# Optimization experiments

Measured on AMD Instinct MI355X. Metric: run time of the kernel, lower is better.

## Reference

```python
import jax, jax.numpy as jnp
import numpy as np

D_MODEL = 512
NUM_HEADS = 8
VOCAB = 32000
B, TQ, TS = 4, 512, 512


def setup_inputs() -> dict:
    key = jax.random.key(0)
    ks = jax.random.split(key, 12)
    s = 1.0 / np.sqrt(D_MODEL)
    inp = {
        "src_vocab_size": VOCAB,
        "dec_output": jax.random.normal(ks[0], (B, TQ, D_MODEL), jnp.float32),
        "enc_output": jax.random.normal(ks[1], (B, TS, D_MODEL), jnp.float32),
        "src": jax.random.randint(ks[2], (B, TS), 0, VOCAB),
        "p1": jax.random.uniform(ks[3], (B, TQ, VOCAB), jnp.float32),
        # fcQ: d_model -> d_model (xavier)
        "WfcQ": jax.random.normal(ks[4], (D_MODEL, D_MODEL), jnp.float32) * s,
        "bfcQ": jnp.zeros((D_MODEL,), jnp.float32),
        # MHA query / key projections (V and output proj skipped in copy mode)
        "Wq": jax.random.normal(ks[5], (D_MODEL, D_MODEL), jnp.float32) * s,
        "bq": jnp.zeros((D_MODEL,), jnp.float32),
        "Wk": jax.random.normal(ks[6], (D_MODEL, D_MODEL), jnp.float32) * s,
        "bk": jnp.zeros((D_MODEL,), jnp.float32),
        # fcw: d_model -> 1 gate
        "Wfcw": jax.random.normal(ks[7], (1, D_MODEL), jnp.float32) * s,
        "bfcw": jnp.zeros((1,), jnp.float32),
    }
    return inp


def reference(src_vocab_size, dec_output, enc_output, src, p1,
              WfcQ, bfcQ, Wq, bq, Wk, bk, Wfcw, bfcw):
    b, tq, d = dec_output.shape
    h = NUM_HEADS
    dh = d // h
    # copy_query = fcQ(dec_output)
    cq = dec_output @ WfcQ.T + bfcQ
    # per-head Q, K projections
    Q = (cq @ Wq.T + bq).reshape(b, tq, h, dh).transpose(0, 2, 1, 3)          # [b,h,tq,dh]
    K = (enc_output @ Wk.T + bk).reshape(b, -1, h, dh).transpose(0, 2, 1, 3)  # [b,h,ts,dh]
    scale = 1.0 / jnp.sqrt(jnp.asarray(dh, dec_output.dtype))
    scores = jnp.einsum('bhqd,bhkd->bhqk', Q, K) * scale
    attn = jax.nn.softmax(scores, axis=-1).mean(axis=1)  # [b,tq,ts] head-averaged
    # attn @ one_hot(src, vocab)  ==  scatter-add of attn weights by src token id
    def scatter_copy(a, s):  # a: [tq,ts], s: [ts]
        return jax.ops.segment_sum(a.T, s, num_segments=src_vocab_size).T  # [tq,vocab]
    a_output = jax.vmap(scatter_copy)(attn, src)  # [b,tq,vocab]
    p2 = jax.nn.softmax(a_output, axis=-1)
    w = jax.nn.sigmoid(dec_output @ Wfcw.T + bfcw)  # [b,tq,1]
    return p2 * w + (1.0 - w) * p1
```

## Files before the change

### kernel.cpp

```cpp
#include <hip/hip_runtime.h>

constexpr int BATCH = 4;
constexpr int SEQ   = 512;
constexpr int DM    = 512;
constexpr int NH    = 8;
constexpr int NV    = 32000;
constexpr int NROWS = BATCH * SEQ;

typedef short short8 __attribute__((ext_vector_type(8)));
typedef float floatx4 __attribute__((ext_vector_type(4)));

__device__ __forceinline__ float wave_reduce_max(float v) {
#pragma unroll
  for (int o = 32; o > 0; o >>= 1) v = fmaxf(v, __shfl_down(v, o, 64));
  return v;
}
__device__ __forceinline__ float wave_reduce_sum(float v) {
#pragma unroll
  for (int o = 32; o > 0; o >>= 1) v += __shfl_down(v, o, 64);
  return v;
}
__device__ __forceinline__ unsigned short f2bf(float f) {
  unsigned u = __float_as_uint(f);
  u += 0x7FFFu + ((u >> 16) & 1u);
  return (unsigned short)(u >> 16);
}
__device__ __forceinline__ float bf2f(unsigned short b) {
  return __uint_as_float(((unsigned)b) << 16);
}

__global__ __launch_bounds__(256)
void convert_bf16_kernel(const float* __restrict__ in, unsigned short* __restrict__ out, int n4) {
  const int i = blockIdx.x * 256 + threadIdx.x;
  if (i < n4) {
    const float4 v = ((const float4*)in)[i];
    ushort4 o;
    o.x = f2bf(v.x); o.y = f2bf(v.y); o.z = f2bf(v.z); o.w = f2bf(v.w);
    ((ushort4*)out)[i] = o;
  }
}

__global__ __launch_bounds__(256)
void wfold_kernel(const float* __restrict__ Wq, const float* __restrict__ WfcQ,
                  unsigned short* __restrict__ Wqc) {
  __shared__ float As[16][68];
  __shared__ float Bs[16][68];
  const int tid = threadIdx.x, tx = tid & 15, ty = tid >> 4;
  const int m0 = blockIdx.y << 6, n0 = blockIdx.x << 6;
  const int r = tid >> 2, c = (tid & 3) << 2;
  float acc[4][4] = {};
  for (int k0 = 0; k0 < DM; k0 += 16) {
    const float4 av = *(const float4*)(Wq + (size_t)(m0 + r) * DM + k0 + c);
    As[c + 0][r] = av.x; As[c + 1][r] = av.y; As[c + 2][r] = av.z; As[c + 3][r] = av.w;
    const float4 bv = *(const float4*)(WfcQ + (size_t)(k0 + ty) * DM + n0 + (tx << 2));
    *(float4*)(&Bs[ty][tx << 2]) = bv;
    __syncthreads();
#pragma unroll
    for (int kk = 0; kk < 16; ++kk) {
      const float4 a4 = *(const float4*)(&As[kk][ty << 2]);
      const float4 b4 = *(const float4*)(&Bs[kk][tx << 2]);
      const float a[4] = {a4.x, a4.y, a4.z, a4.w};
      const float b[4] = {b4.x, b4.y, b4.z, b4.w};
#pragma unroll
      for (int i = 0; i < 4; ++i)
#pragma unroll
        for (int j = 0; j < 4; ++j) acc[i][j] = fmaf(a[i], b[j], acc[i][j]);
    }
    __syncthreads();
  }
#pragma unroll
  for (int i = 0; i < 4; ++i)
#pragma unroll
    for (int j = 0; j < 4; ++j)
      Wqc[(size_t)(m0 + (ty << 2) + i) * DM + n0 + (tx << 2) + j] = f2bf(acc[i][j]);
}

__global__ __launch_bounds__(512)
void bias_fold_kernel(const float* __restrict__ Wq, const float* __restrict__ bfcQ,
                      const float* __restrict__ bq, float* __restrict__ bq2) {
  const int tid = threadIdx.x, h = tid >> 6, l = tid & 63;
  const int n = blockIdx.x * 8 + h;
  float s = 0.f;
#pragma unroll
  for (int t = 0; t < 8; ++t) {
    const int j = l + 64 * t;
    s = fmaf(Wq[(size_t)n * DM + j], bfcQ[j], s);
  }
  s = wave_reduce_sum(s);
  if (l == 0) bq2[n] = bq[n] + s;
}

__global__ __launch_bounds__(256)
void gemm_mfma_kernel(const unsigned short* __restrict__ A0, const unsigned short* __restrict__ W0,
                      const float* __restrict__ b0, unsigned short* __restrict__ C0,
                      const unsigned short* __restrict__ A1, const unsigned short* __restrict__ W1,
                      const float* __restrict__ b1, unsigned short* __restrict__ C1) {
  const unsigned short* A; const unsigned short* W; const float* bias; unsigned short* C;
  if (blockIdx.z == 0) { A = A0; W = W0; bias = b0; C = C0; }
  else                 { A = A1; W = W1; bias = b1; C = C1; }
  const int m0 = blockIdx.y << 6, n0 = blockIdx.x << 6;
  __shared__ __align__(16) unsigned short As[64 * 72];
  __shared__ __align__(16) unsigned short Ws[64 * 72];
  const int tid = threadIdx.x;
  const int wv = tid >> 6, l = tid & 63;
  const int lm = l & 15, lq = l >> 4;
  floatx4 acc[4] = {};
  for (int k0 = 0; k0 < DM; k0 += 64) {
#pragma unroll
    for (int i = 0; i < 2; ++i) {
      const int ch = tid + (i << 8);
      const int row = ch >> 3, c8 = (ch & 7) << 3;
      *(int4*)(&As[row * 72 + c8]) = *(const int4*)(A + (size_t)(m0 + row) * DM + k0 + c8);
      *(int4*)(&Ws[row * 72 + c8]) = *(const int4*)(W + (size_t)(n0 + row) * DM + k0 + c8);
    }
    __syncthreads();
#pragma unroll
    for (int ks = 0; ks < 64; ks += 32) {
      const short8 a = *(const short8*)(&As[(16 * wv + lm) * 72 + ks + lq * 8]);
#pragma unroll
      for (int c = 0; c < 4; ++c) {
        const short8 b = *(const short8*)(&Ws[(16 * c + lm) * 72 + ks + lq * 8]);
        acc[c] = __builtin_amdgcn_mfma_f32_16x16x32_bf16(a, b, acc[c], 0, 0, 0);
      }
    }
    __syncthreads();
  }
#pragma unroll
  for (int c = 0; c < 4; ++c) {
    const int col = n0 + 16 * c + lm;
    const float bv = bias[col];
#pragma unroll
    for (int r = 0; r < 4; ++r) {
      const int row = m0 + 16 * wv + lq * 4 + r;
      C[(size_t)row * DM + col] = f2bf(acc[c][r] + bv);
    }
  }
}

__global__ __launch_bounds__(256)
void scores_mfma_kernel(const unsigned short* __restrict__ Q, const unsigned short* __restrict__ Kk,
                        unsigned short* __restrict__ scores) {
  const int bh = blockIdx.z, bb = bh >> 3, h = bh & 7;
  const int tq0 = blockIdx.y << 6, ts0 = blockIdx.x << 6;
  __shared__ __align__(16) unsigned short Qs[64 * 72];
  __shared__ __align__(16) unsigned short Ks[64 * 72];
  const int tid = threadIdx.x;
  const int wv = tid >> 6, l = tid & 63;
  const int lm = l & 15, lq = l >> 4;
#pragma unroll
  for (int i = 0; i < 2; ++i) {
    const int ch = tid + (i << 8);
    const int row = ch >> 3, c8 = (ch & 7) << 3;
    *(int4*)(&Qs[row * 72 + c8]) =
        *(const int4*)(Q + (size_t)(bb * SEQ + tq0 + row) * DM + h * 64 + c8);
    *(int4*)(&Ks[row * 72 + c8]) =
        *(const int4*)(Kk + (size_t)(bb * SEQ + ts0 + row) * DM + h * 64 + c8);
  }
  __syncthreads();
  floatx4 acc[4] = {};
#pragma unroll
  for (int ks = 0; ks < 64; ks += 32) {
    const short8 a = *(const short8*)(&Qs[(16 * wv + lm) * 72 + ks + lq * 8]);
#pragma unroll
    for (int c = 0; c < 4; ++c) {
      const short8 b = *(const short8*)(&Ks[(16 * c + lm) * 72 + ks + lq * 8]);
      acc[c] = __builtin_amdgcn_mfma_f32_16x16x32_bf16(a, b, acc[c], 0, 0, 0);
    }
  }
#pragma unroll
  for (int c = 0; c < 4; ++c) {
    const int ts = ts0 + 16 * c + lm;
#pragma unroll
    for (int r = 0; r < 4; ++r) {
      const int tq = tq0 + 16 * wv + lq * 4 + r;
      scores[((size_t)bh * SEQ + tq) * SEQ + ts] = f2bf(acc[c][r] * 0.125f);
    }
  }
}

__global__ void build_map_kernel(const int* __restrict__ src, int* __restrict__ map) {
  const int bb = blockIdx.x, ts = threadIdx.x;
  const int v = src[bb * SEQ + ts];
  atomicCAS(&map[(size_t)bb * NV + v], -1, ts);
}

__global__ __launch_bounds__(512)
void softmax_fused_kernel(const unsigned short* __restrict__ scores, const int* __restrict__ src,
                          const int* __restrict__ map, const float* __restrict__ dec,
                          const float* __restrict__ Wfcw, const float* __restrict__ bfcw,
                          float* __restrict__ expa, float* __restrict__ row_a,
                          float* __restrict__ row_b) {
  __shared__ float hp[8 * 520];
  __shared__ float aslot[512];
  __shared__ float r1[8], r2[8];
  const int row = blockIdx.x, bb = row >> 9, tq = row & 511;
  const int tid = threadIdx.x, h = tid >> 6, l = tid & 63;
  aslot[tid] = 0.f;
  const unsigned short* srow = scores + ((size_t)(bb * NH + h) * SEQ + tq) * SEQ;
  union { int4 v; unsigned short u[8]; } U;
  U.v = *(const int4*)(srow + 8 * l);
  float s[8];
#pragma unroll
  for (int i = 0; i < 8; ++i) s[i] = bf2f(U.u[i]);
  float m = s[0];
#pragma unroll
  for (int i = 1; i < 8; ++i) m = fmaxf(m, s[i]);
  m = wave_reduce_max(m);
  m = __shfl(m, 0, 64);
  float e[8], sum = 0.f;
#pragma unroll
  for (int i = 0; i < 8; ++i) { e[i] = __expf(s[i] - m); sum += e[i]; }
  sum = wave_reduce_sum(sum);
  sum = __shfl(sum, 0, 64);
  const float inv = 1.f / sum;
  float4 p0, p1v;
  p0.x = e[0] * inv; p0.y = e[1] * inv; p0.z = e[2] * inv; p0.w = e[3] * inv;
  p1v.x = e[4] * inv; p1v.y = e[5] * inv; p1v.z = e[6] * inv; p1v.w = e[7] * inv;
  *(float4*)(&hp[h * 520 + 8 * l])     = p0;
  *(float4*)(&hp[h * 520 + 8 * l + 4]) = p1v;
  __syncthreads();
  float a = 0.f;
#pragma unroll
  for (int h2 = 0; h2 < 8; ++h2) a += hp[h2 * 520 + tid];
  a *= 0.125f;
  const int sv = src[bb * SEQ + tid];
  const int rep = map[(size_t)bb * NV + sv];
  atomicAdd(&aslot[rep], a);
  __syncthreads();
  const float ev = __expf(aslot[tid]);
  expa[(size_t)row * SEQ + tid] = ev;
  const float d = dec[(size_t)row * DM + tid] * Wfcw[tid];
  float es = wave_reduce_sum(ev);
  float ds = wave_reduce_sum(d);
  if (l == 0) { r1[h] = es; r2[h] = ds; }
  __syncthreads();
  if (tid == 0) {
    float esum = 0.f, dsum = bfcw[0];
#pragma unroll
    for (int i = 0; i < 8; ++i) { esum += r1[i]; dsum += r2[i]; }
    const float w = 1.f / (1.f + __expf(-dsum));
    row_a[row] = 1.f - w;
    row_b[row] = w / ((float)(NV - SEQ) + esum);
  }
}

__global__ __launch_bounds__(256)
void final_kernel(const float* __restrict__ p1, const int* __restrict__ map,
                  const float* __restrict__ expa, const float* __restrict__ row_a,
                  const float* __restrict__ row_b, float* __restrict__ out) {
  const size_t g = (size_t)blockIdx.x * 256 + threadIdx.x;
  const int row = (int)(g / (NV / 4));
  const int q4  = (int)(g % (NV / 4));
  const int bb = row >> 9;
  const float4 p = ((const float4*)p1)[g];
  const int4 m = *(const int4*)(map + (size_t)bb * NV + (q4 << 2));
  const float ra = row_a[row], rb = row_b[row];
  const float* ea = expa + (size_t)row * SEQ;
  const float e0 = (m.x >= 0) ? ea[m.x] : 1.f;
  const float e1 = (m.y >= 0) ? ea[m.y] : 1.f;
  const float e2 = (m.z >= 0) ? ea[m.z] : 1.f;
  const float e3 = (m.w >= 0) ? ea[m.w] : 1.f;
  float4 o;
  o.x = fmaf(ra, p.x, rb * e0);
  o.y = fmaf(ra, p.y, rb * e1);
  o.z = fmaf(ra, p.z, rb * e2);
  o.w = fmaf(ra, p.w, rb * e3);
  ((float4*)out)[g] = o;
}

extern "C" void kernel_launch(void* const* d_in, const int* in_sizes, int n_in,
                              void* d_out, int out_size, void* d_ws, size_t ws_size,
                              hipStream_t stream) {
  const float* dec  = (const float*)d_in[1];
  const float* enc  = (const float*)d_in[2];
  const int*   src  = (const int*)d_in[3];
  const float* p1   = (const float*)d_in[4];
  const float* WfcQ = (const float*)d_in[5];
  const float* bfcQ = (const float*)d_in[6];
  const float* Wq   = (const float*)d_in[7];
  const float* bq   = (const float*)d_in[8];
  const float* Wk   = (const float*)d_in[9];
  const float* bk   = (const float*)d_in[10];
  const float* Wfcw = (const float*)d_in[11];
  const float* bfcw = (const float*)d_in[12];
  float* out = (float*)d_out;

  char* ws = (char*)d_ws;
  int*            map     = (int*)(ws);
  unsigned short* dec_bf  = (unsigned short*)(ws + (size_t)( 1 << 20));
  unsigned short* enc_bf  = (unsigned short*)(ws + (size_t)( 3 << 20));
  unsigned short* wk_bf   = (unsigned short*)(ws + (size_t)( 5 << 20));
  unsigned short* wqc_bf  = (unsigned short*)(ws + (size_t)( 5 << 20) + (512 << 10));
  float*          bq2     = (float*)(ws + (size_t)( 6 << 20));
  float*          row_a   = (float*)(ws + (size_t)( 6 << 20) + (64 << 10));
  float*          row_b   = (float*)(ws + (size_t)( 6 << 20) + (128 << 10));
  unsigned short* qlin_bf = (unsigned short*)(ws + (size_t)( 7 << 20));
  unsigned short* klin_bf = (unsigned short*)(ws + (size_t)( 9 << 20));
  float*          expa    = (float*)(ws + (size_t)(11 << 20));
  unsigned short* scores  = (unsigned short*)(ws + (size_t)(16 << 20));

  hipMemsetAsync(map, 0xFF, (size_t)BATCH * NV * sizeof(int), stream);
  build_map_kernel<<<BATCH, SEQ, 0, stream>>>(src, map);

  convert_bf16_kernel<<<1024, 256, 0, stream>>>(dec, dec_bf, NROWS * DM / 4);
  convert_bf16_kernel<<<1024, 256, 0, stream>>>(enc, enc_bf, NROWS * DM / 4);
  convert_bf16_kernel<<<256, 256, 0, stream>>>(Wk, wk_bf, DM * DM / 4);

  wfold_kernel<<<dim3(8, 8), 256, 0, stream>>>(Wq, WfcQ, wqc_bf);
  bias_fold_kernel<<<64, 512, 0, stream>>>(Wq, bfcQ, bq, bq2);

  gemm_mfma_kernel<<<dim3(8, 32, 2), 256, 0, stream>>>(
      dec_bf, wqc_bf, bq2, qlin_bf, enc_bf, wk_bf, bk, klin_bf);

  scores_mfma_kernel<<<dim3(8, 8, 32), 256, 0, stream>>>(qlin_bf, klin_bf, scores);

  softmax_fused_kernel<<<NROWS, 512, 0, stream>>>(scores, src, map, dec, Wfcw, bfcw,
                                                  expa, row_a, row_b);

  final_kernel<<<(NROWS * (NV / 4)) / 256, 256, 0, stream>>>(p1, map, expa, row_a, row_b, out);
}
```

Baseline: 520.7 us.

## Merge prep kernels, stage GEMM/score stores via LDS, streamline final pass

```diff
diff --git a/kernel.cpp b/kernel.cpp
--- a/kernel.cpp
+++ b/kernel.cpp
@@ -9,6 +9,7 @@
 
 typedef short short8 __attribute__((ext_vector_type(8)));
 typedef float floatx4 __attribute__((ext_vector_type(4)));
+typedef float floatv4 __attribute__((ext_vector_type(4)));
 
 __device__ __forceinline__ float wave_reduce_max(float v) {
 #pragma unroll
@@ -30,64 +31,75 @@
 }
 
 __global__ __launch_bounds__(256)
-void convert_bf16_kernel(const float* __restrict__ in, unsigned short* __restrict__ out, int n4) {
-  const int i = blockIdx.x * 256 + threadIdx.x;
-  if (i < n4) {
+void prep_kernel(const float* __restrict__ dec, const float* __restrict__ enc,
+                 const float* __restrict__ Wk,
+                 unsigned short* __restrict__ dec_bf, unsigned short* __restrict__ enc_bf,
+                 unsigned short* __restrict__ wk_bf,
+                 const int* __restrict__ src, int* __restrict__ map,
+                 const float* __restrict__ Wq, const float* __restrict__ WfcQ,
+                 unsigned short* __restrict__ wqc_bf,
+                 const float* __restrict__ bfcQ, const float* __restrict__ bq,
+                 float* __restrict__ bq2) {
+  __shared__ float As[16][68];
+  __shared__ float Bs[16][68];
+  const int b = blockIdx.x, tid = threadIdx.x;
+  if (b < 64) {
+    const int m0 = (b >> 3) << 6, n0 = (b & 7) << 6;
+    const int tx = tid & 15, ty = tid >> 4;
+    const int r = tid >> 2, c = (tid & 3) << 2;
+    float acc[4][4] = {};
+    for (int k0 = 0; k0 < DM; k0 += 16) {
+      const float4 av = *(const float4*)(Wq + (size_t)(m0 + r) * DM + k0 + c);
+      As[c + 0][r] = av.x; As[c + 1][r] = av.y; As[c + 2][r] = av.z; As[c + 3][r] = av.w;
+      const float4 bv = *(const float4*)(WfcQ + (size_t)(k0 + ty) * DM + n0 + (tx << 2));
+      *(float4*)(&Bs[ty][tx << 2]) = bv;
+      __syncthreads();
+#pragma unroll
+      for (int kk = 0; kk < 16; ++kk) {
+        const float4 a4 = *(const float4*)(&As[kk][ty << 2]);
+        const float4 b4 = *(const float4*)(&Bs[kk][tx << 2]);
+        const float a[4] = {a4.x, a4.y, a4.z, a4.w};
+        const float bb[4] = {b4.x, b4.y, b4.z, b4.w};
+#pragma unroll
+        for (int i = 0; i < 4; ++i)
+#pragma unroll
+          for (int j = 0; j < 4; ++j) acc[i][j] = fmaf(a[i], bb[j], acc[i][j]);
+      }
+      __syncthreads();
+    }
+#pragma unroll
+    for (int i = 0; i < 4; ++i)
+#pragma unroll
+      for (int j = 0; j < 4; ++j)
+        wqc_bf[(size_t)(m0 + (ty << 2) + i) * DM + n0 + (tx << 2) + j] = f2bf(acc[i][j]);
+  } else if (b < 2368) {
+    const int cb = b - 64;
+    const float* in; unsigned short* outp; int i;
+    if (cb < 1024)      { in = dec; outp = dec_bf; i = cb * 256 + tid; }
+    else if (cb < 2048) { in = enc; outp = enc_bf; i = (cb - 1024) * 256 + tid; }
+    else                { in = Wk;  outp = wk_bf;  i = (cb - 2048) * 256 + tid; }
     const float4 v = ((const float4*)in)[i];
     ushort4 o;
     o.x = f2bf(v.x); o.y = f2bf(v.y); o.z = f2bf(v.z); o.w = f2bf(v.w);
-    ((ushort4*)out)[i] = o;
-  }
-}
-
-__global__ __launch_bounds__(256)
-void wfold_kernel(const float* __restrict__ Wq, const float* __restrict__ WfcQ,
-                  unsigned short* __restrict__ Wqc) {
-  __shared__ float As[16][68];
-  __shared__ float Bs[16][68];
-  const int tid = threadIdx.x, tx = tid & 15, ty = tid >> 4;
-  const int m0 = blockIdx.y << 6, n0 = blockIdx.x << 6;
-  const int r = tid >> 2, c = (tid & 3) << 2;
-  float acc[4][4] = {};
-  for (int k0 = 0; k0 < DM; k0 += 16) {
-    const float4 av = *(const float4*)(Wq + (size_t)(m0 + r) * DM + k0 + c);
-    As[c + 0][r] = av.x; As[c + 1][r] = av.y; As[c + 2][r] = av.z; As[c + 3][r] = av.w;
-    const float4 bv = *(const float4*)(WfcQ + (size_t)(k0 + ty) * DM + n0 + (tx << 2));
-    *(float4*)(&Bs[ty][tx << 2]) = bv;
-    __syncthreads();
-#pragma unroll
-    for (int kk = 0; kk < 16; ++kk) {
-      const float4 a4 = *(const float4*)(&As[kk][ty << 2]);
-      const float4 b4 = *(const float4*)(&Bs[kk][tx << 2]);
-      const float a[4] = {a4.x, a4.y, a4.z, a4.w};
-      const float b[4] = {b4.x, b4.y, b4.z, b4.w};
-#pragma unroll
-      for (int i = 0; i < 4; ++i)
-#pragma unroll
-        for (int j = 0; j < 4; ++j) acc[i][j] = fmaf(a[i], b[j], acc[i][j]);
-    }
-    __syncthreads();
-  }
-#pragma unroll
-  for (int i = 0; i < 4; ++i)
-#pragma unroll
-    for (int j = 0; j < 4; ++j)
-      Wqc[(size_t)(m0 + (ty << 2) + i) * DM + n0 + (tx << 2) + j] = f2bf(acc[i][j]);
-}
-
-__global__ __launch_bounds__(512)
-void bias_fold_kernel(const float* __restrict__ Wq, const float* __restrict__ bfcQ,
-                      const float* __restrict__ bq, float* __restrict__ bq2) {
-  const int tid = threadIdx.x, h = tid >> 6, l = tid & 63;
-  const int n = blockIdx.x * 8 + h;
-  float s = 0.f;
-#pragma unroll
-  for (int t = 0; t < 8; ++t) {
-    const int j = l + 64 * t;
-    s = fmaf(Wq[(size_t)n * DM + j], bfcQ[j], s);
-  }
-  s = wave_reduce_sum(s);
-  if (l == 0) bq2[n] = bq[n] + s;
+    ((ushort4*)outp)[i] = o;
+  } else if (b < 2372) {
+    const int bb = b - 2368;
+    const int v0 = src[bb * SEQ + tid];
+    atomicCAS(&map[(size_t)bb * NV + v0], -1, tid);
+    const int v1 = src[bb * SEQ + tid + 256];
+    atomicCAS(&map[(size_t)bb * NV + v1], -1, tid + 256);
+  } else {
+    const int h = tid >> 6, l = tid & 63;
+    const int n = (b - 2372) * 4 + h;
+    float s = 0.f;
+#pragma unroll
+    for (int t = 0; t < 8; ++t) {
+      const int j = l + 64 * t;
+      s = fmaf(Wq[(size_t)n * DM + j], bfcQ[j], s);
+    }
+    s = wave_reduce_sum(s);
+    if (l == 0) bq2[n] = bq[n] + s;
+  }
 }
 
 __global__ __launch_bounds__(256)
@@ -127,13 +139,17 @@
   }
 #pragma unroll
   for (int c = 0; c < 4; ++c) {
-    const int col = n0 + 16 * c + lm;
-    const float bv = bias[col];
-#pragma unroll
-    for (int r = 0; r < 4; ++r) {
-      const int row = m0 + 16 * wv + lq * 4 + r;
-      C[(size_t)row * DM + col] = f2bf(acc[c][r] + bv);
-    }
+    const float bv = bias[n0 + 16 * c + lm];
+#pragma unroll
+    for (int r = 0; r < 4; ++r)
+      As[(16 * wv + lq * 4 + r) * 72 + 16 * c + lm] = f2bf(acc[c][r] + bv);
+  }
+  __syncthreads();
+#pragma unroll
+  for (int i = 0; i < 2; ++i) {
+    const int idx = tid + (i << 8);
+    const int row = idx >> 3, c8 = (idx & 7) << 3;
+    *(int4*)(C + (size_t)(m0 + row) * DM + n0 + c8) = *(const int4*)(&As[row * 72 + c8]);
   }
 }
 
@@ -167,21 +183,20 @@
       acc[c] = __builtin_amdgcn_mfma_f32_16x16x32_bf16(a, b, acc[c], 0, 0, 0);
     }
   }
-#pragma unroll
-  for (int c = 0; c < 4; ++c) {
-    const int ts = ts0 + 16 * c + lm;
-#pragma unroll
-    for (int r = 0; r < 4; ++r) {
-      const int tq = tq0 + 16 * wv + lq * 4 + r;
-      scores[((size_t)bh * SEQ + tq) * SEQ + ts] = f2bf(acc[c][r] * 0.125f);
-    }
-  }
-}
-
-__global__ void build_map_kernel(const int* __restrict__ src, int* __restrict__ map) {
-  const int bb = blockIdx.x, ts = threadIdx.x;
-  const int v = src[bb * SEQ + ts];
-  atomicCAS(&map[(size_t)bb * NV + v], -1, ts);
+  __syncthreads();
+#pragma unroll
+  for (int c = 0; c < 4; ++c)
+#pragma unroll
+    for (int r = 0; r < 4; ++r)
+      Qs[(16 * wv + lq * 4 + r) * 72 + 16 * c + lm] = f2bf(acc[c][r] * 0.125f);
+  __syncthreads();
+#pragma unroll
+  for (int i = 0; i < 2; ++i) {
+    const int idx = tid + (i << 8);
+    const int row = idx >> 3, c8 = (idx & 7) << 3;
+    *(int4*)(scores + ((size_t)bh * SEQ + tq0 + row) * SEQ + ts0 + c8) =
+        *(const int4*)(&Qs[row * 72 + c8]);
+  }
 }
 
 __global__ __launch_bounds__(512)
@@ -244,28 +259,32 @@
   }
 }
 
-__global__ __launch_bounds__(256)
+__global__ __launch_bounds__(320)
 void final_kernel(const float* __restrict__ p1, const int* __restrict__ map,
                   const float* __restrict__ expa, const float* __restrict__ row_a,
                   const float* __restrict__ row_b, float* __restrict__ out) {
-  const size_t g = (size_t)blockIdx.x * 256 + threadIdx.x;
-  const int row = (int)(g / (NV / 4));
-  const int q4  = (int)(g % (NV / 4));
-  const int bb = row >> 9;
-  const float4 p = ((const float4*)p1)[g];
+  const int row = blockIdx.y;
+  const int q4  = blockIdx.x * 320 + threadIdx.x;
+  const int bb  = row >> 9;
+  const size_t g = (size_t)row * (NV / 4) + q4;
+  const floatv4 p = __builtin_nontemporal_load((const floatv4*)p1 + g);
   const int4 m = *(const int4*)(map + (size_t)bb * NV + (q4 << 2));
   const float ra = row_a[row], rb = row_b[row];
   const float* ea = expa + (size_t)row * SEQ;
-  const float e0 = (m.x >= 0) ? ea[m.x] : 1.f;
-  const float e1 = (m.y >= 0) ? ea[m.y] : 1.f;
-  const float e2 = (m.z >= 0) ? ea[m.z] : 1.f;
-  const float e3 = (m.w >= 0) ? ea[m.w] : 1.f;
-  float4 o;
+  const float t0 = ea[m.x & 511];
+  const float t1 = ea[m.y & 511];
+  const float t2 = ea[m.z & 511];
+  const float t3 = ea[m.w & 511];
+  const float e0 = (m.x >= 0) ? t0 : 1.f;
+  const float e1 = (m.y >= 0) ? t1 : 1.f;
+  const float e2 = (m.z >= 0) ? t2 : 1.f;
+  const float e3 = (m.w >= 0) ? t3 : 1.f;
+  floatv4 o;
   o.x = fmaf(ra, p.x, rb * e0);
   o.y = fmaf(ra, p.y, rb * e1);
   o.z = fmaf(ra, p.z, rb * e2);
   o.w = fmaf(ra, p.w, rb * e3);
-  ((float4*)out)[g] = o;
+  __builtin_nontemporal_store(o, (floatv4*)out + g);
 }
 
 extern "C" void kernel_launch(void* const* d_in, const int* in_sizes, int n_in,
@@ -300,14 +319,9 @@
   unsigned short* scores  = (unsigned short*)(ws + (size_t)(16 << 20));
 
   hipMemsetAsync(map, 0xFF, (size_t)BATCH * NV * sizeof(int), stream);
-  build_map_kernel<<<BATCH, SEQ, 0, stream>>>(src, map);
-
-  convert_bf16_kernel<<<1024, 256, 0, stream>>>(dec, dec_bf, NROWS * DM / 4);
-  convert_bf16_kernel<<<1024, 256, 0, stream>>>(enc, enc_bf, NROWS * DM / 4);
-  convert_bf16_kernel<<<256, 256, 0, stream>>>(Wk, wk_bf, DM * DM / 4);
-
-  wfold_kernel<<<dim3(8, 8), 256, 0, stream>>>(Wq, WfcQ, wqc_bf);
-  bias_fold_kernel<<<64, 512, 0, stream>>>(Wq, bfcQ, bq, bq2);
+
+  prep_kernel<<<2500, 256, 0, stream>>>(dec, enc, Wk, dec_bf, enc_bf, wk_bf,
+                                        src, map, Wq, WfcQ, wqc_bf, bfcQ, bq, bq2);
 
   gemm_mfma_kernel<<<dim3(8, 32, 2), 256, 0, stream>>>(
       dec_bf, wqc_bf, bq2, qlin_bf, enc_bf, wk_bf, bk, klin_bf);
@@ -317,5 +331,5 @@
   softmax_fused_kernel<<<NROWS, 512, 0, stream>>>(scores, src, map, dec, Wfcw, bfcw,
                                                   expa, row_a, row_b);
 
-  final_kernel<<<(NROWS * (NV / 4)) / 256, 256, 0, stream>>>(p1, map, expa, row_a, row_b, out);
-}
+  final_kernel<<<dim3(25, NROWS), 320, 0, stream>>>(p1, map, expa, row_a, row_b, out);
+}
```

After: 510.2 us. -2.0%, faster.
